# Performance work log

Measured on AMD Instinct MI355X. Metric: run time of the kernel, lower is better.

The kernel has to match this reference:

```python
import jax, jax.numpy as jnp
import numpy as np

NUM_GRAPHS = 500
BN_EPS = 1e-5


def setup_inputs() -> dict:
    key = jax.random.key(0)
    ks = jax.random.split(key, 16)
    N, E, F, D, L = 100000, 1600000, 128, 128, 3
    x = jax.random.normal(ks[0], (N, F), dtype=jnp.float32)
    edge_index = jax.random.randint(ks[1], (2, E), 0, N)
    batch = jnp.sort(jax.random.randint(ks[2], (N,), 0, NUM_GRAPHS))
    s = 1.0 / np.sqrt(F)
    sd = 1.0 / np.sqrt(D)
    # SAGEConv layer 0: out = lin_l(mean_aggr(x_j)) + lin_r(x)
    sage_Wl = jax.random.uniform(ks[3], (F, D), jnp.float32, -s, s)
    sage_bl = jax.random.uniform(ks[4], (D,), jnp.float32, -s, s)
    sage_Wr = jax.random.uniform(ks[5], (F, D), jnp.float32, -s, s)
    # GINConv layers 1..L-1: nn = Linear(D,D) -> ReLU -> Linear(D,D)
    gin_W1 = jax.random.uniform(ks[6], (L - 1, D, D), jnp.float32, -sd, sd)
    gin_b1 = jax.random.uniform(ks[7], (L - 1, D), jnp.float32, -sd, sd)
    gin_W2 = jax.random.uniform(ks[8], (L - 1, D, D), jnp.float32, -sd, sd)
    gin_b2 = jax.random.uniform(ks[9], (L - 1, D), jnp.float32, -sd, sd)
    bn_gamma = jnp.ones((L, D), dtype=jnp.float32)
    bn_beta = jnp.zeros((L, D), dtype=jnp.float32)
    return {"x": x, "edge_index": edge_index, "batch": batch,
            "sage_Wl": sage_Wl, "sage_bl": sage_bl, "sage_Wr": sage_Wr,
            "gin_W1": gin_W1, "gin_b1": gin_b1, "gin_W2": gin_W2, "gin_b2": gin_b2,
            "bn_gamma": bn_gamma, "bn_beta": bn_beta}


def _batchnorm(h, gamma, beta):
    mu = jnp.mean(h, axis=0)
    var = jnp.var(h, axis=0)  # biased, as torch BN uses for normalization
    return (h - mu) * jax.lax.rsqrt(var + BN_EPS) * gamma + beta


def reference(x, edge_index, batch, sage_Wl, sage_bl, sage_Wr,
              gin_W1, gin_b1, gin_W2, gin_b2, bn_gamma, bn_beta):
    N = x.shape[0]
    src, dst = edge_index[0], edge_index[1]
    L = bn_gamma.shape[0]

    # Layer 0: SAGEConv (mean aggregation, root weight, no bias on lin_r)
    deg = jax.ops.segment_sum(jnp.ones_like(dst, dtype=x.dtype), dst, num_segments=N)
    aggr = jax.ops.segment_sum(x[src], dst, num_segments=N)
    aggr = aggr / jnp.maximum(deg, 1.0)[:, None]
    h = aggr @ sage_Wl + sage_bl + x @ sage_Wr
    h = jax.nn.relu(h)
    h = _batchnorm(h, bn_gamma[0], bn_beta[0])
    xs = [h]

    # Layers 1..L-1: GINConv (eps=0): nn(x + sum_aggr(x_j))
    for i in range(1, L):
        aggr = jax.ops.segment_sum(h[src], dst, num_segments=N)
        t = h + aggr
        t = jax.nn.relu(t @ gin_W1[i - 1] + gin_b1[i - 1])
        t = t @ gin_W2[i - 1] + gin_b2[i - 1]
        h = jax.nn.relu(t)
        h = _batchnorm(h, bn_gamma[i], bn_beta[i])
        xs.append(h)

    # pooling != 'last': concat global_add_pool over every layer
    pooled = jnp.concatenate(
        [jax.ops.segment_sum(xi, batch, num_segments=NUM_GRAPHS) for xi in xs], axis=1)
    node_feats = jnp.concatenate(xs, axis=1)
    return (pooled, node_feats)
```

## Files before the change

### kernel.cpp

```cpp
#include <hip/hip_runtime.h>
#include <hip/hip_bf16.h>


#define BN_EPS 1e-5f
#define EPB 4096

typedef short s8v __attribute__((ext_vector_type(8)));
typedef float f4v __attribute__((ext_vector_type(4)));

__device__ __forceinline__ float bflo(unsigned u) { return __uint_as_float(u << 16); }
__device__ __forceinline__ float bfhi(unsigned u) { return __uint_as_float(u & 0xffff0000u); }
__device__ __forceinline__ unsigned short f2bf(float f) {
    unsigned u = __float_as_uint(f);
    unsigned r = (u + 0x7fffu + ((u >> 16) & 1u)) >> 16;
    return (unsigned short)r;
}
__device__ __forceinline__ unsigned pk2(float a, float b) {
    return (unsigned)f2bf(a) | ((unsigned)f2bf(b) << 16);
}
__device__ __forceinline__ void unpack8(uint4 u, float* v) {
    v[0] = bflo(u.x); v[1] = bfhi(u.x);
    v[2] = bflo(u.y); v[3] = bfhi(u.y);
    v[4] = bflo(u.z); v[5] = bfhi(u.z);
    v[6] = bflo(u.w); v[7] = bfhi(u.w);
}


__global__ __launch_bounds__(256) void k_binA(const int* __restrict__ src,
                                              const int* __restrict__ dst, int E, int NB, int CAP,
                                              int* __restrict__ bcnt,
                                              unsigned long long* __restrict__ ebuf) {
    __shared__ int hist[512], base[512], cur[512];
    const int tid = threadIdx.x;
    const int e0 = blockIdx.x * EPB;
    for (int i = tid; i < 512; i += 256) { hist[i] = 0; cur[i] = 0; }
    __syncthreads();
#pragma unroll
    for (int k = 0; k < EPB / 256; k++) {
        int e = e0 + k * 256 + tid;
        if (e < E) atomicAdd(&hist[dst[e] >> 8], 1);
    }
    __syncthreads();
    for (int b = tid; b < NB; b += 256)
        base[b] = hist[b] ? atomicAdd(&bcnt[b], hist[b]) : 0;
    __syncthreads();
#pragma unroll
    for (int k = 0; k < EPB / 256; k++) {
        int e = e0 + k * 256 + tid;
        if (e < E) {
            int d = dst[e];
            int b = d >> 8;
            int lp = atomicAdd(&cur[b], 1);
            int gp = base[b] + lp;
            if (gp < CAP)
                ebuf[(size_t)b * CAP + gp] = ((unsigned long long)d << 32) | (unsigned)src[e];
        }
    }
}

__global__ void k_bscan(const int* __restrict__ bcnt, int NB, int* __restrict__ bbase) {
    __shared__ int sm[256];
    const int tid = threadIdx.x;
    const int c = (NB + 255) / 256;
    int s = 0;
    for (int k = 0; k < c; k++) { int i = tid * c + k; if (i < NB) s += bcnt[i]; }
    sm[tid] = s;
    __syncthreads();
    for (int off = 1; off < 256; off <<= 1) {
        int v = (tid >= off) ? sm[tid - off] : 0;
        __syncthreads();
        sm[tid] += v;
        __syncthreads();
    }
    int run = sm[tid] - s;
    for (int k = 0; k < c; k++) {
        int i = tid * c + k;
        if (i < NB) { bbase[i] = run; run += bcnt[i]; }
    }
}

__global__ __launch_bounds__(256) void k_binB(const unsigned long long* __restrict__ ebuf,
                                              int CAP, const int* __restrict__ bcnt,
                                              const int* __restrict__ bbase,
                                              int N, int E,
                                              int* __restrict__ rp, int* __restrict__ csr) {
    __shared__ int deg[256], sc[256], cur[256];
    const int tid = threadIdx.x;
    const int b = blockIdx.x;
    const int cnt = min(bcnt[b], CAP);
    const int cbase = bbase[b];
    deg[tid] = 0;
    __syncthreads();
    const unsigned long long* eb = ebuf + (size_t)b * CAP;
    for (int i = tid; i < cnt; i += 256) {
        int d = (int)(eb[i] >> 32);
        atomicAdd(&deg[d & 255], 1);
    }
    __syncthreads();
    int myDeg = deg[tid];
    sc[tid] = myDeg;
    __syncthreads();
    for (int off = 1; off < 256; off <<= 1) {
        int v = (tid >= off) ? sc[tid - off] : 0;
        __syncthreads();
        sc[tid] += v;
        __syncthreads();
    }
    int pos = cbase + sc[tid] - myDeg;
    int node = b * 256 + tid;
    if (node < N) rp[node] = pos;
    cur[tid] = pos;
    __syncthreads();
    for (int i = tid; i < cnt; i += 256) {
        unsigned long long e = eb[i];
        int d = (int)(e >> 32);
        int p = atomicAdd(&cur[d & 255], 1);
        csr[p] = (int)(e & 0xffffffffu);
    }
    if (b == 0 && tid == 0) rp[N] = E;
}


__global__ void k_cvt_bf16(const float* __restrict__ in, uint4* __restrict__ out, int n8) {
    int i = blockIdx.x * 256 + threadIdx.x;
    if (i >= n8) return;
    const float4* p = reinterpret_cast<const float4*>(in) + (size_t)i * 2;
    float4 a = p[0], b = p[1];
    uint4 o;
    o.x = pk2(a.x, a.y); o.y = pk2(a.z, a.w);
    o.z = pk2(b.x, b.y); o.w = pk2(b.z, b.w);
    out[i] = o;
}

__global__ void k_pack_w(const float* __restrict__ W, unsigned short* __restrict__ out) {
    int idx = blockIdx.x * 256 + threadIdx.x;
    int k = idx >> 7, d = idx & 127;
    float w = W[idx];
    unsigned short h = f2bf(w);
    float hf = __uint_as_float((unsigned)h << 16);
    unsigned short l = f2bf(w - hf);
    int o = (((k >> 3) * 128) + d) * 8 + (k & 7);
    out[o] = h;
    out[16384 + o] = l;
}

__global__ void k_cvt_h(const float* __restrict__ y,
                        const float* __restrict__ sa, const float* __restrict__ sc,
                        uint4* __restrict__ out, int N) {
    int idx = blockIdx.x * 256 + threadIdx.x;
    if (idx >= N * 16) return;
    int n = idx >> 4, cc = idx & 15;
    const float* p = y + (size_t)n * 384 + cc * 8;
    float4 x0 = *reinterpret_cast<const float4*>(p);
    float4 x1 = *reinterpret_cast<const float4*>(p + 4);
    const float4 a0 = *reinterpret_cast<const float4*>(sa + cc * 8);
    const float4 a1 = *reinterpret_cast<const float4*>(sa + cc * 8 + 4);
    const float4 c0 = *reinterpret_cast<const float4*>(sc + cc * 8);
    const float4 c1 = *reinterpret_cast<const float4*>(sc + cc * 8 + 4);
    uint4 o;
    o.x = pk2(fmaf(x0.x, a0.x, c0.x), fmaf(x0.y, a0.y, c0.y));
    o.y = pk2(fmaf(x0.z, a0.z, c0.z), fmaf(x0.w, a0.w, c0.w));
    o.z = pk2(fmaf(x1.x, a1.x, c1.x), fmaf(x1.y, a1.y, c1.y));
    o.w = pk2(fmaf(x1.z, a1.z, c1.z), fmaf(x1.w, a1.w, c1.w));
    out[(size_t)n * 16 + cc] = o;
}


template <bool SELF, bool MEAN>
__global__ __launch_bounds__(256) void k_aggr(const int* __restrict__ rp,
                                              const int* __restrict__ csr,
                                              const uint4* __restrict__ src,
                                              uint4* __restrict__ out, int N) {
    const int node = blockIdx.x * 4 + (threadIdx.x >> 6);
    if (node >= N) return;
    const int lane = threadIdx.x & 63;
    const int c = lane & 15, grp = lane >> 4;

    float acc[8];
#pragma unroll
    for (int k = 0; k < 8; k++) acc[k] = 0.f;

    const int lo = rp[node], hi = rp[node + 1];
    int j = lo + grp;
    for (; j + 4 < hi; j += 8) {
        int sn0 = csr[j];
        int sn1 = csr[j + 4];
        uint4 r0 = src[(size_t)sn0 * 16 + c];
        uint4 r1 = src[(size_t)sn1 * 16 + c];
        float v[8];
        unpack8(r0, v);
#pragma unroll
        for (int k = 0; k < 8; k++) acc[k] += v[k];
        unpack8(r1, v);
#pragma unroll
        for (int k = 0; k < 8; k++) acc[k] += v[k];
    }
    if (j < hi) {
        float v[8];
        unpack8(src[(size_t)csr[j] * 16 + c], v);
#pragma unroll
        for (int k = 0; k < 8; k++) acc[k] += v[k];
    }

#pragma unroll
    for (int k = 0; k < 8; k++) {
        acc[k] += __shfl_xor(acc[k], 16, 64);
        acc[k] += __shfl_xor(acc[k], 32, 64);
    }

    if (grp == 0) {
        if (SELF) {
            float v[8];
            unpack8(src[(size_t)node * 16 + c], v);
#pragma unroll
            for (int k = 0; k < 8; k++) acc[k] += v[k];
        }
        if (MEAN) {
            float inv = 1.0f / fmaxf((float)(hi - lo), 1.0f);
#pragma unroll
            for (int k = 0; k < 8; k++) acc[k] *= inv;
        }
        uint4 o;
        o.x = pk2(acc[0], acc[1]); o.y = pk2(acc[2], acc[3]);
        o.z = pk2(acc[4], acc[5]); o.w = pk2(acc[6], acc[7]);
        out[(size_t)node * 16 + c] = o;
    }
}


#define MFMA_STAGE(Whi, Wlo, B0, B1, ACC)                                          \
    _Pragma("unroll")                                                              \
    for (int ks = 0; ks < 4; ks++) {                                               \
        s8v b0 = __builtin_bit_cast(s8v, B0[ks]);                                  \
        s8v b1 = __builtin_bit_cast(s8v, B1[ks]);                                  \
        _Pragma("unroll")                                                          \
        for (int df = 0; df < 8; df++) {                                           \
            int wi = (ks * 4 + lg) * 128 + df * 16 + l16;                          \
            s8v ah = __builtin_bit_cast(s8v, Whi[wi]);                             \
            s8v al = __builtin_bit_cast(s8v, Wlo[wi]);                             \
            ACC[0][df] = __builtin_amdgcn_mfma_f32_16x16x32_bf16(ah, b0, ACC[0][df], 0, 0, 0); \
            ACC[1][df] = __builtin_amdgcn_mfma_f32_16x16x32_bf16(ah, b1, ACC[1][df], 0, 0, 0); \
            ACC[0][df] = __builtin_amdgcn_mfma_f32_16x16x32_bf16(al, b0, ACC[0][df], 0, 0, 0); \
            ACC[1][df] = __builtin_amdgcn_mfma_f32_16x16x32_bf16(al, b1, ACC[1][df], 0, 0, 0); \
        }                                                                          \
    }

#define STATS_EPILOGUE(OO, V0, V1)                                                 \
    {                                                                              \
        _Pragma("unroll")                                                          \
        for (int df = 0; df < 8; df++) {                                           \
            float s[4], q[4];                                                      \
            _Pragma("unroll")                                                      \
            for (int r = 0; r < 4; r++) {                                          \
                float a0 = V0 ? (&OO[0][df].x)[r] : 0.f;                           \
                float a1 = V1 ? (&OO[1][df].x)[r] : 0.f;                           \
                s[r] = a0 + a1;                                                    \
                q[r] = a0 * a0 + a1 * a1;                                          \
            }                                                                      \
            _Pragma("unroll")                                                      \
            for (int m = 1; m < 16; m <<= 1) {                                     \
                _Pragma("unroll")                                                  \
                for (int r = 0; r < 4; r++) {                                      \
                    s[r] += __shfl_xor(s[r], m, 64);                               \
                    q[r] += __shfl_xor(q[r], m, 64);                               \
                }                                                                  \
            }                                                                      \
            if (l16 == 0) {                                                        \
                _Pragma("unroll")                                                  \
                for (int r = 0; r < 4; r++) {                                      \
                    sred[wid][df * 16 + lg * 4 + r][0] = s[r];                     \
                    sred[wid][df * 16 + lg * 4 + r][1] = q[r];                     \
                }                                                                  \
            }                                                                      \
        }                                                                          \
        __syncthreads();                                                           \
        if (tid < 128) {                                                           \
            float s = sred[0][tid][0] + sred[1][tid][0] + sred[2][tid][0] + sred[3][tid][0]; \
            float q = sred[0][tid][1] + sred[1][tid][1] + sred[2][tid][1] + sred[3][tid][1]; \
            unsafeAtomicAdd(&gsum[tid], s);                                        \
            unsafeAtomicAdd(&gsq[tid], q);                                         \
        }                                                                          \
    }


__global__ __launch_bounds__(256) void k_gemm_sage(
    const uint4* __restrict__ A1, const uint4* __restrict__ A2,
    const uint4* __restrict__ Wfrag,
    const float* __restrict__ bias,
    float* __restrict__ outF, float* __restrict__ gsum, float* __restrict__ gsq,
    int N) {
    __shared__ float sred[4][128][2];
    const int tid = threadIdx.x;
    const int lane = tid & 63, wid = tid >> 6;
    const int nbase = blockIdx.x * 128 + wid * 32;
    const int l16 = lane & 15, lg = lane >> 4;

    f4v acc[2][8];
#pragma unroll
    for (int nf = 0; nf < 2; nf++)
#pragma unroll
        for (int df = 0; df < 8; df++)
            acc[nf][df] = (f4v){0.f, 0.f, 0.f, 0.f};

#pragma unroll
    for (int t = 0; t < 2; t++) {
        const uint4* A = t ? A2 : A1;
        const uint4* Whi = Wfrag + (size_t)t * 4096;
        const uint4* Wlo = Whi + 2048;
        uint4 bvec[2][4];
#pragma unroll
        for (int nf = 0; nf < 2; nf++) {
            const uint4* row = A + (size_t)(nbase + nf * 16 + l16) * 16;
#pragma unroll
            for (int ks = 0; ks < 4; ks++) bvec[nf][ks] = row[ks * 4 + lg];
        }
        MFMA_STAGE(Whi, Wlo, bvec[0], bvec[1], acc)
    }

    const bool v0 = (nbase + l16) < N;
    const bool v1 = (nbase + 16 + l16) < N;
    float4 oo[2][8];
#pragma unroll
    for (int df = 0; df < 8; df++) {
        int d0 = df * 16 + lg * 4;
        const float4 bb = *reinterpret_cast<const float4*>(bias + d0);
#pragma unroll
        for (int nf = 0; nf < 2; nf++) {
            oo[nf][df].x = fmaxf(acc[nf][df][0] + bb.x, 0.f);
            oo[nf][df].y = fmaxf(acc[nf][df][1] + bb.y, 0.f);
            oo[nf][df].z = fmaxf(acc[nf][df][2] + bb.z, 0.f);
            oo[nf][df].w = fmaxf(acc[nf][df][3] + bb.w, 0.f);
        }
    }

    STATS_EPILOGUE(oo, v0, v1)

#pragma unroll
    for (int nf = 0; nf < 2; nf++) {
        int n = nbase + nf * 16 + l16;
        if (n < N) {
#pragma unroll
            for (int df = 0; df < 8; df++)
                *reinterpret_cast<float4*>(outF + (size_t)n * 384 + df * 16 + lg * 4) = oo[nf][df];
        }
    }
}


__global__ __launch_bounds__(256) void k_gemm_gin(
    const uint4* __restrict__ A,
    const uint4* __restrict__ W1f, const uint4* __restrict__ W2f,
    const float* __restrict__ b1, const float* __restrict__ b2,
    float* __restrict__ outF, float* __restrict__ gsum, float* __restrict__ gsq,
    int N) {
    __shared__ uint4 tile[2048];
    __shared__ float sred[4][128][2];
    const int tid = threadIdx.x;
    const int lane = tid & 63, wid = tid >> 6;
    const int nbase = blockIdx.x * 128 + wid * 32;
    const int l16 = lane & 15, lg = lane >> 4;

    f4v acc[2][8];
#pragma unroll
    for (int nf = 0; nf < 2; nf++)
#pragma unroll
        for (int df = 0; df < 8; df++)
            acc[nf][df] = (f4v){0.f, 0.f, 0.f, 0.f};

    {
        const uint4* Whi = W1f;
        const uint4* Wlo = W1f + 2048;
        uint4 bvec[2][4];
#pragma unroll
        for (int nf = 0; nf < 2; nf++) {
            const uint4* row = A + (size_t)(nbase + nf * 16 + l16) * 16;
#pragma unroll
            for (int ks = 0; ks < 4; ks++) bvec[nf][ks] = row[ks * 4 + lg];
        }
        MFMA_STAGE(Whi, Wlo, bvec[0], bvec[1], acc)
    }
#pragma unroll
    for (int df = 0; df < 8; df++) {
        int d0 = df * 16 + lg * 4;
        const float4 bb = *reinterpret_cast<const float4*>(b1 + d0);
#pragma unroll
        for (int nf = 0; nf < 2; nf++) {
            float tx = fmaxf(acc[nf][df][0] + bb.x, 0.f);
            float ty = fmaxf(acc[nf][df][1] + bb.y, 0.f);
            float tz = fmaxf(acc[nf][df][2] + bb.z, 0.f);
            float tw = fmaxf(acc[nf][df][3] + bb.w, 0.f);
            uint2 p;
            p.x = pk2(tx, ty);
            p.y = pk2(tz, tw);
            int row = wid * 32 + nf * 16 + l16;
            int col4 = df * 2 + (lg >> 1);
            int slot = row * 16 + (col4 ^ (row & 15));
            *reinterpret_cast<uint2*>(
                reinterpret_cast<char*>(tile) + (size_t)slot * 16 + (lg & 1) * 8) = p;
        }
    }
    __syncthreads();

#pragma unroll
    for (int nf = 0; nf < 2; nf++)
#pragma unroll
        for (int df = 0; df < 8; df++)
            acc[nf][df] = (f4v){0.f, 0.f, 0.f, 0.f};
    {
        const uint4* Whi = W2f;
        const uint4* Wlo = W2f + 2048;
        uint4 bvec[2][4];
#pragma unroll
        for (int nf = 0; nf < 2; nf++) {
            int row = wid * 32 + nf * 16 + l16;
#pragma unroll
            for (int ks = 0; ks < 4; ks++)
                bvec[nf][ks] = tile[row * 16 + ((ks * 4 + lg) ^ (row & 15))];
        }
        MFMA_STAGE(Whi, Wlo, bvec[0], bvec[1], acc)
    }

    const bool v0 = (nbase + l16) < N;
    const bool v1 = (nbase + 16 + l16) < N;
    float4 oo[2][8];
#pragma unroll
    for (int df = 0; df < 8; df++) {
        int d0 = df * 16 + lg * 4;
        const float4 bb = *reinterpret_cast<const float4*>(b2 + d0);
#pragma unroll
        for (int nf = 0; nf < 2; nf++) {
            oo[nf][df].x = fmaxf(acc[nf][df][0] + bb.x, 0.f);
            oo[nf][df].y = fmaxf(acc[nf][df][1] + bb.y, 0.f);
            oo[nf][df].z = fmaxf(acc[nf][df][2] + bb.z, 0.f);
            oo[nf][df].w = fmaxf(acc[nf][df][3] + bb.w, 0.f);
        }
    }

    STATS_EPILOGUE(oo, v0, v1)

#pragma unroll
    for (int nf = 0; nf < 2; nf++) {
        int n = nbase + nf * 16 + l16;
        if (n < N) {
#pragma unroll
            for (int df = 0; df < 8; df++)
                *reinterpret_cast<float4*>(outF + (size_t)n * 384 + df * 16 + lg * 4) = oo[nf][df];
        }
    }
}


__global__ void k_bnfin(float* __restrict__ gsum, float* __restrict__ gsq,
                        const float* __restrict__ gamma, const float* __restrict__ beta,
                        int N, float* __restrict__ a, float* __restrict__ c) {
    int d = threadIdx.x;
    float invN = 1.0f / (float)N;
    float mu = gsum[d] * invN;
    float var = gsq[d] * invN - mu * mu;
    float rs = rsqrtf(var + BN_EPS);
    float aa = gamma[d] * rs;
    a[d] = aa;
    c[d] = beta[d] - mu * aa;
    gsum[d] = 0.f;
    gsq[d] = 0.f;
}


__global__ __launch_bounds__(384) void k_finpool(float* __restrict__ nf,
                                                 const float* __restrict__ a3,
                                                 const float* __restrict__ c3,
                                                 const int* __restrict__ batch,
                                                 int N, float* __restrict__ pooled) {
    const int d = threadIdx.x;
    const float a = a3[d], c = c3[d];
    const int n0 = blockIdx.x * 64;
    const int n1 = min(n0 + 64, N);
    float s = 0.f;
    int curg = batch[n0];
    for (int n = n0; n < n1; n++) {
        int g = batch[n];
        if (g != curg) {
            unsafeAtomicAdd(&pooled[(size_t)curg * 384 + d], s);
            s = 0.f;
            curg = g;
        }
        float v = nf[(size_t)n * 384 + d];
        float h = fmaf(v, a, c);
        nf[(size_t)n * 384 + d] = h;
        s += h;
    }
    unsafeAtomicAdd(&pooled[(size_t)curg * 384 + d], s);
}


extern "C" void kernel_launch(void* const* d_in, const int* in_sizes, int n_in,
                              void* d_out, int out_size, void* d_ws, size_t ws_size,
                              hipStream_t stream) {
    const float* x   = (const float*)d_in[0];
    const int*   ei  = (const int*)d_in[1];
    const int*   bat = (const int*)d_in[2];
    const float* sWl = (const float*)d_in[3];
    const float* sbl = (const float*)d_in[4];
    const float* sWr = (const float*)d_in[5];
    const float* gW1 = (const float*)d_in[6];
    const float* gb1 = (const float*)d_in[7];
    const float* gW2 = (const float*)d_in[8];
    const float* gb2 = (const float*)d_in[9];
    const float* bng = (const float*)d_in[10];
    const float* bnb = (const float*)d_in[11];

    const int N = in_sizes[0] / 128;
    const int E = in_sizes[1] / 2;
    const int G = out_size / 384 - N;
    const int* srcp = ei;
    const int* dstp = ei + E;

    char* w = (char*)d_ws;
    auto alloc = [&](size_t bytes) -> void* {
        void* p = (void*)w;
        w += (bytes + 255) & ~(size_t)255;
        return p;
    };
    const size_t Npad = (size_t)(N + 128);
    int*   rp    = (int*)alloc(((size_t)N + 1) * 4);
    int*   csr   = (int*)alloc((size_t)E * 4);
    int*   bcnt  = (int*)alloc(8192);
    int*   bbase = (int*)alloc(8192);
    float* gsum  = (float*)alloc(512);
    float* gsq   = (float*)alloc(512);
    float* abuf  = (float*)alloc(3 * 512);
    float* cbuf  = (float*)alloc(3 * 512);
    unsigned short* Wp = (unsigned short*)alloc((size_t)6 * 2 * 16384 * 2);
    unsigned short* ab = (unsigned short*)alloc(Npad * 256);
    unsigned short* tb = (unsigned short*)alloc(Npad * 256);

    float* pooled = (float*)d_out;
    float* nf     = pooled + (size_t)G * 384;

    const int NB  = (N + 255) / 256;
    int CAP = ((2 * (E / (NB > 0 ? NB : 1)) + 511) / 512) * 512;
    const long long maxcap = (long long)(Npad * 256) / ((long long)NB * 8);
    if ((long long)CAP > maxcap) CAP = (int)(maxcap & ~511LL);
    unsigned long long* ebuf = (unsigned long long*)ab;

    const int egrid = (E + EPB - 1) / EPB;
    const int agrid = (N + 3) / 4;
    const int ggrid = (N + 127) / 128;
    const int vgrid = (N * 16 + 255) / 256;
    const int fgrid = (N + 63) / 64;

    hipMemsetAsync(bcnt, 0, (size_t)NB * 4, stream);
    k_binA<<<egrid, 256, 0, stream>>>(srcp, dstp, E, NB, CAP, bcnt, ebuf);
    k_bscan<<<1, 256, 0, stream>>>(bcnt, NB, bbase);
    k_binB<<<NB, 256, 0, stream>>>(ebuf, CAP, bcnt, bbase, N, E, rp, csr);

    k_cvt_bf16<<<vgrid, 256, 0, stream>>>(x, (uint4*)tb, N * 16);
    k_pack_w<<<64, 256, 0, stream>>>(sWl,         Wp + 0 * 32768);
    k_pack_w<<<64, 256, 0, stream>>>(sWr,         Wp + 1 * 32768);
    k_pack_w<<<64, 256, 0, stream>>>(gW1,         Wp + 2 * 32768);
    k_pack_w<<<64, 256, 0, stream>>>(gW2,         Wp + 3 * 32768);
    k_pack_w<<<64, 256, 0, stream>>>(gW1 + 16384, Wp + 4 * 32768);
    k_pack_w<<<64, 256, 0, stream>>>(gW2 + 16384, Wp + 5 * 32768);
    hipMemsetAsync(gsum, 0, 1024, stream);
    hipMemsetAsync(pooled, 0, (size_t)G * 384 * 4, stream);

    k_aggr<false, true><<<agrid, 256, 0, stream>>>(rp, csr, (const uint4*)tb, (uint4*)ab, N);
    k_gemm_sage<<<ggrid, 256, 0, stream>>>(
        (const uint4*)ab, (const uint4*)tb, (const uint4*)Wp, sbl, nf, gsum, gsq, N);
    k_bnfin<<<1, 128, 0, stream>>>(gsum, gsq, bng, bnb, N, abuf, cbuf);
    k_cvt_h<<<vgrid, 256, 0, stream>>>(nf, abuf, cbuf, (uint4*)tb, N);

    for (int l = 1; l < 3; l++) {
        const uint4* W1p = (const uint4*)(Wp + (size_t)(2 * l) * 32768);
        const uint4* W2p = (const uint4*)(Wp + (size_t)(2 * l + 1) * 32768);
        const float* b1 = gb1 + (size_t)(l - 1) * 128;
        const float* b2 = gb2 + (size_t)(l - 1) * 128;
        float* nfl = nf + (size_t)l * 128;

        k_aggr<true, false><<<agrid, 256, 0, stream>>>(rp, csr, (const uint4*)tb, (uint4*)ab, N);
        k_gemm_gin<<<ggrid, 256, 0, stream>>>(
            (const uint4*)ab, W1p, W2p, b1, b2, nfl, gsum, gsq, N);
        k_bnfin<<<1, 128, 0, stream>>>(gsum, gsq, bng + l * 128, bnb + l * 128, N,
                                       abuf + (size_t)l * 128, cbuf + (size_t)l * 128);
        if (l < 2)
            k_cvt_h<<<vgrid, 256, 0, stream>>>(nfl, abuf + (size_t)l * 128,
                                               cbuf + (size_t)l * 128, (uint4*)tb, N);
    }

    k_finpool<<<fgrid, 384, 0, stream>>>(nf, abuf, cbuf, bat, N, pooled);
}
```

Baseline: 591.3 us.

## Cut kernel launches by folding scan, BN finalize and weight packing into other kernels

Removes the separate block-scan kernel by having each k_binB block reduce the preceding bucket counts itself. Drops the three k_bnfin launches by computing BN scale and shift inline in k_cvt_h and k_finpool from per-layer stat buffers, and merges the six weight-pack launches into one. The per-layer stat buffers share one zeroed region, so two memsets are folded into one. The aggregation loop also gains a 4-way unrolled gather path for more loads in flight. The cost is redundant work: binB does an O(NB) prefix sum per block, and cvt_h recomputes BN constants in every thread.

```diff
diff --git a/kernel.cpp b/kernel.cpp
--- a/kernel.cpp
+++ b/kernel.cpp
@@ -58,37 +58,28 @@
     }
 }
 
-__global__ void k_bscan(const int* __restrict__ bcnt, int NB, int* __restrict__ bbase) {
-    __shared__ int sm[256];
-    const int tid = threadIdx.x;
-    const int c = (NB + 255) / 256;
-    int s = 0;
-    for (int k = 0; k < c; k++) { int i = tid * c + k; if (i < NB) s += bcnt[i]; }
-    sm[tid] = s;
-    __syncthreads();
-    for (int off = 1; off < 256; off <<= 1) {
-        int v = (tid >= off) ? sm[tid - off] : 0;
-        __syncthreads();
-        sm[tid] += v;
-        __syncthreads();
-    }
-    int run = sm[tid] - s;
-    for (int k = 0; k < c; k++) {
-        int i = tid * c + k;
-        if (i < NB) { bbase[i] = run; run += bcnt[i]; }
-    }
-}
-
 __global__ __launch_bounds__(256) void k_binB(const unsigned long long* __restrict__ ebuf,
                                               int CAP, const int* __restrict__ bcnt,
-                                              const int* __restrict__ bbase,
                                               int N, int E,
                                               int* __restrict__ rp, int* __restrict__ csr) {
     __shared__ int deg[256], sc[256], cur[256];
+    __shared__ int s_cbase;
     const int tid = threadIdx.x;
     const int b = blockIdx.x;
     const int cnt = min(bcnt[b], CAP);
-    const int cbase = bbase[b];
+
+    int partial = 0;
+    for (int i = tid; i < b; i += 256) partial += bcnt[i];
+    sc[tid] = partial;
+    __syncthreads();
+    for (int off = 128; off > 0; off >>= 1) {
+        if (tid < off) sc[tid] += sc[tid + off];
+        __syncthreads();
+    }
+    if (tid == 0) s_cbase = sc[0];
+    __syncthreads();
+    const int cbase = s_cbase;
+
     deg[tid] = 0;
     __syncthreads();
     const unsigned long long* eb = ebuf + (size_t)b * CAP;
@@ -132,36 +123,58 @@
     out[i] = o;
 }
 
-__global__ void k_pack_w(const float* __restrict__ W, unsigned short* __restrict__ out) {
-    int idx = blockIdx.x * 256 + threadIdx.x;
+__global__ void k_pack_all(const float* __restrict__ sWl, const float* __restrict__ sWr,
+                           const float* __restrict__ gW1, const float* __restrict__ gW2,
+                           unsigned short* __restrict__ out) {
+    int gid = blockIdx.x;
+    int wsel = gid >> 6;
+    int idx = (gid & 63) * 256 + threadIdx.x;
+    const float* W;
+    switch (wsel) {
+        case 0: W = sWl; break;
+        case 1: W = sWr; break;
+        case 2: W = gW1; break;
+        case 3: W = gW2; break;
+        case 4: W = gW1 + 16384; break;
+        default: W = gW2 + 16384; break;
+    }
     int k = idx >> 7, d = idx & 127;
     float w = W[idx];
     unsigned short h = f2bf(w);
     float hf = __uint_as_float((unsigned)h << 16);
     unsigned short l = f2bf(w - hf);
     int o = (((k >> 3) * 128) + d) * 8 + (k & 7);
-    out[o] = h;
-    out[16384 + o] = l;
+    unsigned short* slot = out + (size_t)wsel * 32768;
+    slot[o] = h;
+    slot[16384 + o] = l;
 }
 
 __global__ void k_cvt_h(const float* __restrict__ y,
-                        const float* __restrict__ sa, const float* __restrict__ sc,
-                        uint4* __restrict__ out, int N) {
+                        const float* __restrict__ gsumL, const float* __restrict__ gsqL,
+                        const float* __restrict__ gamma, const float* __restrict__ beta,
+                        float invN, uint4* __restrict__ out, int N) {
     int idx = blockIdx.x * 256 + threadIdx.x;
     if (idx >= N * 16) return;
     int n = idx >> 4, cc = idx & 15;
+    float av[8], cv[8];
+#pragma unroll
+    for (int k = 0; k < 8; k++) {
+        int d = cc * 8 + k;
+        float mu = gsumL[d] * invN;
+        float var = gsqL[d] * invN - mu * mu;
+        float rs = rsqrtf(var + BN_EPS);
+        float aa = gamma[d] * rs;
+        av[k] = aa;
+        cv[k] = beta[d] - mu * aa;
+    }
     const float* p = y + (size_t)n * 384 + cc * 8;
     float4 x0 = *reinterpret_cast<const float4*>(p);
     float4 x1 = *reinterpret_cast<const float4*>(p + 4);
-    const float4 a0 = *reinterpret_cast<const float4*>(sa + cc * 8);
-    const float4 a1 = *reinterpret_cast<const float4*>(sa + cc * 8 + 4);
-    const float4 c0 = *reinterpret_cast<const float4*>(sc + cc * 8);
-    const float4 c1 = *reinterpret_cast<const float4*>(sc + cc * 8 + 4);
     uint4 o;
-    o.x = pk2(fmaf(x0.x, a0.x, c0.x), fmaf(x0.y, a0.y, c0.y));
-    o.y = pk2(fmaf(x0.z, a0.z, c0.z), fmaf(x0.w, a0.w, c0.w));
-    o.z = pk2(fmaf(x1.x, a1.x, c1.x), fmaf(x1.y, a1.y, c1.y));
-    o.w = pk2(fmaf(x1.z, a1.z, c1.z), fmaf(x1.w, a1.w, c1.w));
+    o.x = pk2(fmaf(x0.x, av[0], cv[0]), fmaf(x0.y, av[1], cv[1]));
+    o.y = pk2(fmaf(x0.z, av[2], cv[2]), fmaf(x0.w, av[3], cv[3]));
+    o.z = pk2(fmaf(x1.x, av[4], cv[4]), fmaf(x1.y, av[5], cv[5]));
+    o.w = pk2(fmaf(x1.z, av[6], cv[6]), fmaf(x1.w, av[7], cv[7]));
     out[(size_t)n * 16 + cc] = o;
 }
 
@@ -182,6 +195,29 @@
 
     const int lo = rp[node], hi = rp[node + 1];
     int j = lo + grp;
+    for (; j + 12 < hi; j += 16) {
+        int sn0 = csr[j];
+        int sn1 = csr[j + 4];
+        int sn2 = csr[j + 8];
+        int sn3 = csr[j + 12];
+        uint4 r0 = src[(size_t)sn0 * 16 + c];
+        uint4 r1 = src[(size_t)sn1 * 16 + c];
+        uint4 r2 = src[(size_t)sn2 * 16 + c];
+        uint4 r3 = src[(size_t)sn3 * 16 + c];
+        float v[8];
+        unpack8(r0, v);
+#pragma unroll
+        for (int k = 0; k < 8; k++) acc[k] += v[k];
+        unpack8(r1, v);
+#pragma unroll
+        for (int k = 0; k < 8; k++) acc[k] += v[k];
+        unpack8(r2, v);
+#pragma unroll
+        for (int k = 0; k < 8; k++) acc[k] += v[k];
+        unpack8(r3, v);
+#pragma unroll
+        for (int k = 0; k < 8; k++) acc[k] += v[k];
+    }
     for (; j + 4 < hi; j += 8) {
         int sn0 = csr[j];
         int sn1 = csr[j + 4];
@@ -450,29 +486,21 @@
 }
 
 
-__global__ void k_bnfin(float* __restrict__ gsum, float* __restrict__ gsq,
-                        const float* __restrict__ gamma, const float* __restrict__ beta,
-                        int N, float* __restrict__ a, float* __restrict__ c) {
-    int d = threadIdx.x;
-    float invN = 1.0f / (float)N;
+__global__ __launch_bounds__(384) void k_finpool(float* __restrict__ nf,
+                                                 const float* __restrict__ gsum,
+                                                 const float* __restrict__ gsq,
+                                                 const float* __restrict__ gamma,
+                                                 const float* __restrict__ beta,
+                                                 float invN,
+                                                 const int* __restrict__ batch,
+                                                 int N, float* __restrict__ pooled) {
+    const int d = threadIdx.x;
     float mu = gsum[d] * invN;
     float var = gsq[d] * invN - mu * mu;
     float rs = rsqrtf(var + BN_EPS);
-    float aa = gamma[d] * rs;
-    a[d] = aa;
-    c[d] = beta[d] - mu * aa;
-    gsum[d] = 0.f;
-    gsq[d] = 0.f;
-}
-
-
-__global__ __launch_bounds__(384) void k_finpool(float* __restrict__ nf,
-                                                 const float* __restrict__ a3,
-                                                 const float* __restrict__ c3,
-                                                 const int* __restrict__ batch,
-                                                 int N, float* __restrict__ pooled) {
-    const int d = threadIdx.x;
-    const float a = a3[d], c = c3[d];
+    const float a = gamma[d] * rs;
+    const float c = beta[d] - mu * a;
+
     const int n0 = blockIdx.x * 64;
     const int n1 = min(n0 + 64, N);
     float s = 0.f;
@@ -524,18 +552,18 @@
     const size_t Npad = (size_t)(N + 128);
     int*   rp    = (int*)alloc(((size_t)N + 1) * 4);
     int*   csr   = (int*)alloc((size_t)E * 4);
-    int*   bcnt  = (int*)alloc(8192);
-    int*   bbase = (int*)alloc(8192);
-    float* gsum  = (float*)alloc(512);
-    float* gsq   = (float*)alloc(512);
-    float* abuf  = (float*)alloc(3 * 512);
-    float* cbuf  = (float*)alloc(3 * 512);
+    char*  zreg  = (char*)alloc(2048 + 2 * 3 * 512);
+    int*   bcnt  = (int*)zreg;
+    float* gsum  = (float*)(zreg + 2048);
+    float* gsq   = gsum + 3 * 128;
     unsigned short* Wp = (unsigned short*)alloc((size_t)6 * 2 * 16384 * 2);
     unsigned short* ab = (unsigned short*)alloc(Npad * 256);
     unsigned short* tb = (unsigned short*)alloc(Npad * 256);
 
     float* pooled = (float*)d_out;
     float* nf     = pooled + (size_t)G * 384;
+
+    const float invN = 1.0f / (float)N;
 
     const int NB  = (N + 255) / 256;
     int CAP = ((2 * (E / (NB > 0 ? NB : 1)) + 511) / 512) * 512;
@@ -549,26 +577,19 @@
     const int vgrid = (N * 16 + 255) / 256;
     const int fgrid = (N + 63) / 64;
 
-    hipMemsetAsync(bcnt, 0, (size_t)NB * 4, stream);
+    hipMemsetAsync(zreg, 0, 2048 + 2 * 3 * 512, stream);
+    hipMemsetAsync(pooled, 0, (size_t)G * 384 * 4, stream);
+
     k_binA<<<egrid, 256, 0, stream>>>(srcp, dstp, E, NB, CAP, bcnt, ebuf);
-    k_bscan<<<1, 256, 0, stream>>>(bcnt, NB, bbase);
-    k_binB<<<NB, 256, 0, stream>>>(ebuf, CAP, bcnt, bbase, N, E, rp, csr);
+    k_binB<<<NB, 256, 0, stream>>>(ebuf, CAP, bcnt, N, E, rp, csr);
 
     k_cvt_bf16<<<vgrid, 256, 0, stream>>>(x, (uint4*)tb, N * 16);
-    k_pack_w<<<64, 256, 0, stream>>>(sWl,         Wp + 0 * 32768);
-    k_pack_w<<<64, 256, 0, stream>>>(sWr,         Wp + 1 * 32768);
-    k_pack_w<<<64, 256, 0, stream>>>(gW1,         Wp + 2 * 32768);
-    k_pack_w<<<64, 256, 0, stream>>>(gW2,         Wp + 3 * 32768);
-    k_pack_w<<<64, 256, 0, stream>>>(gW1 + 16384, Wp + 4 * 32768);
-    k_pack_w<<<64, 256, 0, stream>>>(gW2 + 16384, Wp + 5 * 32768);
-    hipMemsetAsync(gsum, 0, 1024, stream);
-    hipMemsetAsync(pooled, 0, (size_t)G * 384 * 4, stream);
+    k_pack_all<<<6 * 64, 256, 0, stream>>>(sWl, sWr, gW1, gW2, Wp);
 
     k_aggr<false, true><<<agrid, 256, 0, stream>>>(rp, csr, (const uint4*)tb, (uint4*)ab, N);
     k_gemm_sage<<<ggrid, 256, 0, stream>>>(
         (const uint4*)ab, (const uint4*)tb, (const uint4*)Wp, sbl, nf, gsum, gsq, N);
-    k_bnfin<<<1, 128, 0, stream>>>(gsum, gsq, bng, bnb, N, abuf, cbuf);
-    k_cvt_h<<<vgrid, 256, 0, stream>>>(nf, abuf, cbuf, (uint4*)tb, N);
+    k_cvt_h<<<vgrid, 256, 0, stream>>>(nf, gsum, gsq, bng, bnb, invN, (uint4*)tb, N);
 
     for (int l = 1; l < 3; l++) {
         const uint4* W1p = (const uint4*)(Wp + (size_t)(2 * l) * 32768);
@@ -579,13 +600,12 @@
 
         k_aggr<true, false><<<agrid, 256, 0, stream>>>(rp, csr, (const uint4*)tb, (uint4*)ab, N);
         k_gemm_gin<<<ggrid, 256, 0, stream>>>(
-            (const uint4*)ab, W1p, W2p, b1, b2, nfl, gsum, gsq, N);
-        k_bnfin<<<1, 128, 0, stream>>>(gsum, gsq, bng + l * 128, bnb + l * 128, N,
-                                       abuf + (size_t)l * 128, cbuf + (size_t)l * 128);
+            (const uint4*)ab, W1p, W2p, b1, b2, nfl, gsum + l * 128, gsq + l * 128, N);
         if (l < 2)
-            k_cvt_h<<<vgrid, 256, 0, stream>>>(nfl, abuf + (size_t)l * 128,
-                                               cbuf + (size_t)l * 128, (uint4*)tb, N);
-    }
-
-    k_finpool<<<fgrid, 384, 0, stream>>>(nf, abuf, cbuf, bat, N, pooled);
-}
+            k_cvt_h<<<vgrid, 256, 0, stream>>>(nfl, gsum + l * 128, gsq + l * 128,
+                                               bng + l * 128, bnb + l * 128, invN,
+                                               (uint4*)tb, N);
+    }
+
+    k_finpool<<<fgrid, 384, 0, stream>>>(nf, gsum, gsq, bng, bnb, invN, bat, N, pooled);
+}
```

Result: faster. 561.9 us (-5.0%).
